# Performance work log

Hardware: AMD Instinct MI355X
Metric: run time of the kernel (lower is better)

## Reference

```python
import jax, jax.numpy as jnp
import numpy as np

B, N, C, H = 4, 2048, 256, 16
D = C // H  # head dim = 16


def setup_inputs() -> dict:
    key = jax.random.key(0)
    k1, k2, k3 = jax.random.split(key, 3)
    x = jax.random.normal(k1, (B, N, C), dtype=jnp.float32)
    w_qkv = jax.random.normal(k2, (C, 3 * C), dtype=jnp.float32) * (C ** -0.5)
    b_qkv = jnp.zeros((3 * C,), dtype=jnp.float32)
    w_proj = jax.random.normal(k3, (C, C), dtype=jnp.float32) * (C ** -0.5)
    b_proj = jnp.zeros((C,), dtype=jnp.float32)
    return {"x": x, "w_qkv": w_qkv, "b_qkv": b_qkv, "w_proj": w_proj, "b_proj": b_proj}


def reference(x, w_qkv, b_qkv, w_proj, b_proj):
    b, n, c = x.shape
    qkv = x @ w_qkv + b_qkv                       # (B, N, 3C)
    qkv = qkv.reshape(b, n, 3, H, D)
    q = jnp.transpose(qkv[:, :, 0], (0, 2, 1, 3))  # (B, H, N, D)
    k = jnp.transpose(qkv[:, :, 1], (0, 2, 1, 3))
    v = jnp.transpose(qkv[:, :, 2], (0, 2, 1, 3))
    # NOTE: the original module applies NO 1/sqrt(d) scaling.
    attn = jnp.einsum('bhqd,bhkd->bhqk', q, k)     # (B, H, N, N)
    attn = jax.nn.softmax(attn, axis=-1)
    out = jnp.einsum('bhqk,bhkd->bhqd', attn, v)   # (B, H, N, D)
    out = jnp.transpose(out, (0, 2, 1, 3)).reshape(b, n, c)
    return out @ w_proj + b_proj
```

## Files before the change

kernel.cpp:

```cpp
#include <hip/hip_runtime.h>
#include <stdint.h>

typedef __attribute__((ext_vector_type(8))) short short8;
typedef __attribute__((ext_vector_type(4))) short short4v;
typedef __attribute__((ext_vector_type(4))) float float4v;
typedef __attribute__((ext_vector_type(16))) float float16v;
typedef __attribute__((ext_vector_type(4))) uint32_t uint4v;

__device__ __forceinline__ short f2bf(float f) {
    union { float f; uint32_t u; } v; v.f = f;
    uint32_t u = v.u;
    uint32_t r = (u + 0x7fffu + ((u >> 16) & 1u)) >> 16;
    return (short)r;
}

#if __has_builtin(__builtin_amdgcn_cvt_pk_bf16_f32)
typedef __bf16 bf16x2_t __attribute__((ext_vector_type(2)));
__device__ __forceinline__ uint32_t cvt_pk2(float a, float b) {
    union { bf16x2_t v; uint32_t u; } c;
    c.v = __builtin_amdgcn_cvt_pk_bf16_f32(a, b);
    return c.u;
}
#else
__device__ __forceinline__ uint32_t cvt_pk2(float a, float b) {
    union { float f; uint32_t u; } x, y; x.f = a; y.f = b;
    return ((x.u + 0x8000u) >> 16) | ((y.u + 0x8000u) & 0xFFFF0000u);
}
#endif


__global__ __launch_bounds__(256) void cvtW_kernel(const float* __restrict__ wqkv,
                                                   const float* __restrict__ wproj,
                                                   short* __restrict__ outq,
                                                   short* __restrict__ outp) {
    int idx = blockIdx.x * 256 + threadIdx.x;
    if (idx < 196608) {
        int n = idx >> 8, k = idx & 255;
        outq[idx] = f2bf(wqkv[k * 768 + n]);
    } else {
        int i = idx - 196608;
        int n = i >> 8, k = i & 255;
        outp[i] = f2bf(wproj[k * 256 + n]);
    }
}


template<int MODE>
__global__ __launch_bounds__(256) void gemm_kernel(
    const void* __restrict__ Ap, const short* __restrict__ Bt,
    const float* __restrict__ bias,
    short* __restrict__ outQ, short* __restrict__ outK, short* __restrict__ outV,
    float* __restrict__ outP)
{
    const int K = 256;
    int m0 = blockIdx.x * 64;
    int n0 = blockIdx.y * 64;
    int tid = threadIdx.x;
    int wave = tid >> 6, lane = tid & 63, quad = lane >> 4, lc = lane & 15;

    __shared__ __align__(16) short As[64 * 48];
    __shared__ __align__(16) short Bs[64 * 48];

    float4v acc[4];
    #pragma unroll
    for (int t = 0; t < 4; ++t) acc[t] = (float4v){0.f, 0.f, 0.f, 0.f};

    int srow = tid >> 2, sseg = tid & 3;

    for (int c = 0; c < K; c += 32) {
        __syncthreads();
        if (MODE == 0) {
            const float* src = (const float*)Ap + (size_t)(m0 + srow) * K + c + sseg * 8;
            float4 f0 = *(const float4*)src;
            float4 f1 = *(const float4*)(src + 4);
            uint4v u; u.x = cvt_pk2(f0.x, f0.y); u.y = cvt_pk2(f0.z, f0.w);
            u.z = cvt_pk2(f1.x, f1.y); u.w = cvt_pk2(f1.z, f1.w);
            *(uint4v*)(&As[srow * 48 + sseg * 8]) = u;
        } else {
            *(short8*)(&As[srow * 48 + sseg * 8]) =
                *(const short8*)((const short*)Ap + (size_t)(m0 + srow) * K + c + sseg * 8);
        }
        *(short8*)(&Bs[srow * 48 + sseg * 8]) =
            *(const short8*)(Bt + (size_t)(n0 + srow) * K + c + sseg * 8);
        __syncthreads();

        short8 af = *(short8*)(&As[(wave * 16 + lc) * 48 + quad * 8]);
        #pragma unroll
        for (int t = 0; t < 4; ++t) {
            short8 bf = *(short8*)(&Bs[(t * 16 + lc) * 48 + quad * 8]);
            acc[t] = __builtin_amdgcn_mfma_f32_16x16x32_bf16(af, bf, acc[t], 0, 0, 0);
        }
    }

    #pragma unroll
    for (int t = 0; t < 4; ++t) {
        int cg = n0 + t * 16 + lc;
        float bv = bias[cg];
        #pragma unroll
        for (int r = 0; r < 4; ++r) {
            int rg = m0 + wave * 16 + quad * 4 + r;
            float val = acc[t][r] + bv;
            if (MODE == 0) {
                int s = cg >> 8, rem = cg & 255, h = rem >> 4, d = rem & 15;
                int b = rg >> 11, n = rg & 2047;
                if (s == 0) val *= 1.4426950408889634f;
                short* dst = (s == 0) ? outQ : ((s == 1) ? outK : outV);
                dst[((((size_t)b * 16 + h) * 2048 + n) << 4) + d] = f2bf(val);
            } else {
                outP[(size_t)rg * 256 + cg] = val;
            }
        }
    }
}


__global__ __launch_bounds__(256) void attn_kernel(
    const short* __restrict__ Q, const short* __restrict__ Kp, const short* __restrict__ V,
    short* __restrict__ Out)
{
    const int N = 2048;
    int bh = blockIdx.y;
    int b = bh >> 4, h = bh & 15;
    int tid = threadIdx.x;
    int wave = tid >> 6, lane = tid & 63;
    int m = lane & 31, hi = lane >> 5;
    int qbase = blockIdx.x * 128 + wave * 32;

    const short* Qh = Q + (size_t)bh * N * 16;
    const short* Kh = Kp + (size_t)bh * N * 16;
    const short* Vh = V + (size_t)bh * N * 16;

    __shared__ __align__(16) short Vt[32][264];

    {
        int r = 16 + (tid >> 4);
        int c0 = (tid & 15) * 16;
        short fill = (r == 16) ? (short)0x3F80 : (short)0;
        short8 f8;
        #pragma unroll
        for (int j = 0; j < 8; ++j) f8[j] = fill;
        *(short8*)(&Vt[r][c0]) = f8;
        *(short8*)(&Vt[r][c0 + 8]) = f8;
    }

    short8 qf = *(const short8*)(Qh + (size_t)(qbase + m) * 16 + hi * 8);

    float16v Oacc, zf;
    #pragma unroll
    for (int j = 0; j < 16; ++j) { Oacc[j] = 0.f; zf[j] = 0.f; }

    int sd = tid & 15, sa = tid >> 4;
    int kb = ((sa & 1) << 3) | (((sa >> 1) & 1) << 2) | ((sa >> 2) << 4);

    for (int sc = 0; sc < N; sc += 256) {
        __syncthreads();
        #pragma unroll
        for (int cc = 0; cc < 4; ++cc) {
            const short* vp = Vh + (size_t)(sc + cc * 64 + kb) * 16 + sd;
            short4v pack;
            pack.x = vp[0]; pack.y = vp[16]; pack.z = vp[32]; pack.w = vp[48];
            *(short4v*)(&Vt[sd][cc * 64 + sa * 4]) = pack;
        }
        __syncthreads();

        #pragma unroll
        for (int it = 0; it < 4; ++it) {
            int c = sc + it * 64;
            short8 kf1 = *(const short8*)(Kh + (size_t)(c + m) * 16 + hi * 8);
            short8 kf2 = *(const short8*)(Kh + (size_t)(c + 32 + m) * 16 + hi * 8);

            float16v S1 = __builtin_amdgcn_mfma_f32_32x32x16_bf16(kf1, qf, zf, 0, 0, 0);
            float16v S2 = __builtin_amdgcn_mfma_f32_32x32x16_bf16(kf2, qf, zf, 0, 0, 0);

            union { uint4v u; short8 s; } pA, pB, pC, pD;
            pA.u = (uint4v){
                cvt_pk2(__builtin_amdgcn_exp2f(S1[0]), __builtin_amdgcn_exp2f(S1[1])),
                cvt_pk2(__builtin_amdgcn_exp2f(S1[2]), __builtin_amdgcn_exp2f(S1[3])),
                cvt_pk2(__builtin_amdgcn_exp2f(S1[4]), __builtin_amdgcn_exp2f(S1[5])),
                cvt_pk2(__builtin_amdgcn_exp2f(S1[6]), __builtin_amdgcn_exp2f(S1[7]))};
            pB.u = (uint4v){
                cvt_pk2(__builtin_amdgcn_exp2f(S1[8]),  __builtin_amdgcn_exp2f(S1[9])),
                cvt_pk2(__builtin_amdgcn_exp2f(S1[10]), __builtin_amdgcn_exp2f(S1[11])),
                cvt_pk2(__builtin_amdgcn_exp2f(S1[12]), __builtin_amdgcn_exp2f(S1[13])),
                cvt_pk2(__builtin_amdgcn_exp2f(S1[14]), __builtin_amdgcn_exp2f(S1[15]))};
            pC.u = (uint4v){
                cvt_pk2(__builtin_amdgcn_exp2f(S2[0]), __builtin_amdgcn_exp2f(S2[1])),
                cvt_pk2(__builtin_amdgcn_exp2f(S2[2]), __builtin_amdgcn_exp2f(S2[3])),
                cvt_pk2(__builtin_amdgcn_exp2f(S2[4]), __builtin_amdgcn_exp2f(S2[5])),
                cvt_pk2(__builtin_amdgcn_exp2f(S2[6]), __builtin_amdgcn_exp2f(S2[7]))};
            pD.u = (uint4v){
                cvt_pk2(__builtin_amdgcn_exp2f(S2[8]),  __builtin_amdgcn_exp2f(S2[9])),
                cvt_pk2(__builtin_amdgcn_exp2f(S2[10]), __builtin_amdgcn_exp2f(S2[11])),
                cvt_pk2(__builtin_amdgcn_exp2f(S2[12]), __builtin_amdgcn_exp2f(S2[13])),
                cvt_pk2(__builtin_amdgcn_exp2f(S2[14]), __builtin_amdgcn_exp2f(S2[15]))};

            #pragma unroll
            for (int p = 0; p < 4; ++p) {
                short8 vf = *(const short8*)(&Vt[m][it * 64 + p * 16 + hi * 8]);
                short8 pf = (p == 0) ? pA.s : (p == 1) ? pB.s : (p == 2) ? pC.s : pD.s;
                Oacc = __builtin_amdgcn_mfma_f32_32x32x16_bf16(vf, pf, Oacc, 0, 0, 0);
            }
        }
    }

    float Lq = __shfl(Oacc[8], m, 64);
    float inv = 1.0f / Lq;
    uint32_t o0 = cvt_pk2(Oacc[0] * inv, Oacc[1] * inv);
    uint32_t o1 = cvt_pk2(Oacc[2] * inv, Oacc[3] * inv);
    uint32_t o2 = cvt_pk2(Oacc[4] * inv, Oacc[5] * inv);
    uint32_t o3 = cvt_pk2(Oacc[6] * inv, Oacc[7] * inv);
    short* row = Out + ((size_t)(b * 2048 + qbase + m)) * 256 + h * 16;
    uint2 w0; w0.x = o0; w0.y = o1;
    uint2 w1; w1.x = o2; w1.y = o3;
    *(uint2*)(row + hi * 4) = w0;
    *(uint2*)(row + 8 + hi * 4) = w1;
}


extern "C" void kernel_launch(void* const* d_in, const int* in_sizes, int n_in,
                              void* d_out, int out_size, void* d_ws, size_t ws_size,
                              hipStream_t stream) {
    const float* x      = (const float*)d_in[0];
    const float* w_qkv  = (const float*)d_in[1];
    const float* b_qkv  = (const float*)d_in[2];
    const float* w_proj = (const float*)d_in[3];
    const float* b_proj = (const float*)d_in[4];
    float* out = (float*)d_out;

    short* wqkvT  = (short*)d_ws;
    short* wprojT = wqkvT + 196608;
    short* Qb     = wprojT + 65536;
    short* Kb     = Qb + 2097152;
    short* Vb     = Kb + 2097152;
    short* Ab     = Vb + 2097152;

    cvtW_kernel<<<1024, 256, 0, stream>>>(w_qkv, w_proj, wqkvT, wprojT);

    gemm_kernel<0><<<dim3(128, 12), 256, 0, stream>>>(x, wqkvT, b_qkv, Qb, Kb, Vb, nullptr);

    attn_kernel<<<dim3(16, 64), 256, 0, stream>>>(Qb, Kb, Vb, Ab);

    gemm_kernel<1><<<dim3(128, 4), 256, 0, stream>>>(Ab, wprojT, b_proj,
                                                     nullptr, nullptr, nullptr, out);
}
```

Measured before the change: 139.9 us.

## Double GEMM M-tile to 128 rows and shrink attention V shared buffer

The projection GEMMs now compute 128 rows per block, with two 16-row subtiles per wave, so each B-tile load from shared memory is reused across twice as many MFMAs and the grid is halved. Separately, the attention kernel's transposed-V shared buffer drops from 32 to 17 rows: rows 16..31 of the 32x32 MFMA A operand, which held a ones row and zero padding, now all read the single ones row. This cuts LDS footprint and init stores. Rows 17..31 of the output then also accumulate row sums instead of zeros, but they are unused apart from row 16, which supplies the softmax denominator. Fewer GEMM blocks may reduce occupancy on a large-CU device.

```diff
diff --git a/kernel.cpp b/kernel.cpp
--- a/kernel.cpp
+++ b/kernel.cpp
@@ -53,58 +53,69 @@
     float* __restrict__ outP)
 {
     const int K = 256;
-    int m0 = blockIdx.x * 64;
+    int m0 = blockIdx.x * 128;
     int n0 = blockIdx.y * 64;
     int tid = threadIdx.x;
     int wave = tid >> 6, lane = tid & 63, quad = lane >> 4, lc = lane & 15;
 
-    __shared__ __align__(16) short As[64 * 48];
+    __shared__ __align__(16) short As[128 * 48];
     __shared__ __align__(16) short Bs[64 * 48];
 
-    float4v acc[4];
-    #pragma unroll
-    for (int t = 0; t < 4; ++t) acc[t] = (float4v){0.f, 0.f, 0.f, 0.f};
+    float4v acc[2][4];
+    #pragma unroll
+    for (int s = 0; s < 2; ++s)
+        #pragma unroll
+        for (int t = 0; t < 4; ++t) acc[s][t] = (float4v){0.f, 0.f, 0.f, 0.f};
 
     int srow = tid >> 2, sseg = tid & 3;
 
     for (int c = 0; c < K; c += 32) {
         __syncthreads();
-        if (MODE == 0) {
-            const float* src = (const float*)Ap + (size_t)(m0 + srow) * K + c + sseg * 8;
-            float4 f0 = *(const float4*)src;
-            float4 f1 = *(const float4*)(src + 4);
-            uint4v u; u.x = cvt_pk2(f0.x, f0.y); u.y = cvt_pk2(f0.z, f0.w);
-            u.z = cvt_pk2(f1.x, f1.y); u.w = cvt_pk2(f1.z, f1.w);
-            *(uint4v*)(&As[srow * 48 + sseg * 8]) = u;
-        } else {
-            *(short8*)(&As[srow * 48 + sseg * 8]) =
-                *(const short8*)((const short*)Ap + (size_t)(m0 + srow) * K + c + sseg * 8);
+        #pragma unroll
+        for (int s = 0; s < 2; ++s) {
+            int row = srow + s * 64;
+            if (MODE == 0) {
+                const float* src = (const float*)Ap + (size_t)(m0 + row) * K + c + sseg * 8;
+                float4 f0 = *(const float4*)src;
+                float4 f1 = *(const float4*)(src + 4);
+                uint4v u; u.x = cvt_pk2(f0.x, f0.y); u.y = cvt_pk2(f0.z, f0.w);
+                u.z = cvt_pk2(f1.x, f1.y); u.w = cvt_pk2(f1.z, f1.w);
+                *(uint4v*)(&As[row * 48 + sseg * 8]) = u;
+            } else {
+                *(short8*)(&As[row * 48 + sseg * 8]) =
+                    *(const short8*)((const short*)Ap + (size_t)(m0 + row) * K + c + sseg * 8);
+            }
         }
         *(short8*)(&Bs[srow * 48 + sseg * 8]) =
             *(const short8*)(Bt + (size_t)(n0 + srow) * K + c + sseg * 8);
         __syncthreads();
 
-        short8 af = *(short8*)(&As[(wave * 16 + lc) * 48 + quad * 8]);
-        #pragma unroll
-        for (int t = 0; t < 4; ++t) {
-            short8 bf = *(short8*)(&Bs[(t * 16 + lc) * 48 + quad * 8]);
-            acc[t] = __builtin_amdgcn_mfma_f32_16x16x32_bf16(af, bf, acc[t], 0, 0, 0);
-        }
-    }
-
+        #pragma unroll
+        for (int s = 0; s < 2; ++s) {
+            short8 af = *(short8*)(&As[(s * 64 + wave * 16 + lc) * 48 + quad * 8]);
+            #pragma unroll
+            for (int t = 0; t < 4; ++t) {
+                short8 bf = *(short8*)(&Bs[(t * 16 + lc) * 48 + quad * 8]);
+                acc[s][t] = __builtin_amdgcn_mfma_f32_16x16x32_bf16(af, bf, acc[s][t], 0, 0, 0);
+            }
+        }
+    }
+
+    #pragma unroll
+    for (int s = 0; s < 2; ++s)
     #pragma unroll
     for (int t = 0; t < 4; ++t) {
         int cg = n0 + t * 16 + lc;
         float bv = bias[cg];
         #pragma unroll
         for (int r = 0; r < 4; ++r) {
-            int rg = m0 + wave * 16 + quad * 4 + r;
-            float val = acc[t][r] + bv;
+            int rg = m0 + s * 64 + wave * 16 + quad * 4 + r;
+            float val = acc[s][t][r] + bv;
             if (MODE == 0) {
-                int s = cg >> 8, rem = cg & 255, h = rem >> 4, d = rem & 15;
+                int sq = cg >> 8, rem = cg & 255, h = rem >> 4, d = rem & 15;
                 int b = rg >> 11, n = rg & 2047;
-                if (s == 0) val *= 1.4426950408889634f;
-                short* dst = (s == 0) ? outQ : ((s == 1) ? outK : outV);
+                if (sq == 0) val *= 1.4426950408889634f;
+                short* dst = (sq == 0) ? outQ : ((sq == 1) ? outK : outV);
                 dst[((((size_t)b * 16 + h) * 2048 + n) << 4) + d] = f2bf(val);
             } else {
                 outP[(size_t)rg * 256 + cg] = val;
@@ -130,17 +141,14 @@
     const short* Kh = Kp + (size_t)bh * N * 16;
     const short* Vh = V + (size_t)bh * N * 16;
 
-    __shared__ __align__(16) short Vt[32][264];
-
-    {
-        int r = 16 + (tid >> 4);
-        int c0 = (tid & 15) * 16;
-        short fill = (r == 16) ? (short)0x3F80 : (short)0;
+    __shared__ __align__(16) short Vt[17][264];
+
+    if (tid < 16) {
         short8 f8;
         #pragma unroll
-        for (int j = 0; j < 8; ++j) f8[j] = fill;
-        *(short8*)(&Vt[r][c0]) = f8;
-        *(short8*)(&Vt[r][c0 + 8]) = f8;
+        for (int j = 0; j < 8; ++j) f8[j] = (short)0x3F80;
+        *(short8*)(&Vt[16][tid * 16]) = f8;
+        *(short8*)(&Vt[16][tid * 16 + 8]) = f8;
     }
 
     short8 qf = *(const short8*)(Qh + (size_t)(qbase + m) * 16 + hi * 8);
@@ -148,6 +156,8 @@
     float16v Oacc, zf;
     #pragma unroll
     for (int j = 0; j < 16; ++j) { Oacc[j] = 0.f; zf[j] = 0.f; }
+
+    int rEff = (m < 16) ? m : 16;
 
     int sd = tid & 15, sa = tid >> 4;
     int kb = ((sa & 1) << 3) | (((sa >> 1) & 1) << 2) | ((sa >> 2) << 4);
@@ -196,7 +206,7 @@
 
             #pragma unroll
             for (int p = 0; p < 4; ++p) {
-                short8 vf = *(const short8*)(&Vt[m][it * 64 + p * 16 + hi * 8]);
+                short8 vf = *(const short8*)(&Vt[rEff][it * 64 + p * 16 + hi * 8]);
                 short8 pf = (p == 0) ? pA.s : (p == 1) ? pB.s : (p == 2) ? pC.s : pD.s;
                 Oacc = __builtin_amdgcn_mfma_f32_32x32x16_bf16(vf, pf, Oacc, 0, 0, 0);
             }
@@ -236,10 +246,10 @@
 
     cvtW_kernel<<<1024, 256, 0, stream>>>(w_qkv, w_proj, wqkvT, wprojT);
 
-    gemm_kernel<0><<<dim3(128, 12), 256, 0, stream>>>(x, wqkvT, b_qkv, Qb, Kb, Vb, nullptr);
+    gemm_kernel<0><<<dim3(64, 12), 256, 0, stream>>>(x, wqkvT, b_qkv, Qb, Kb, Vb, nullptr);
 
     attn_kernel<<<dim3(16, 64), 256, 0, stream>>>(Qb, Kb, Vb, Ab);
 
-    gemm_kernel<1><<<dim3(128, 4), 256, 0, stream>>>(Ab, wprojT, b_proj,
-                                                     nullptr, nullptr, nullptr, out);
-}
+    gemm_kernel<1><<<dim3(64, 4), 256, 0, stream>>>(Ab, wprojT, b_proj,
+                                                    nullptr, nullptr, nullptr, out);
+}
```

After: 144.0 us. 3.0% more time.

## Keep A rows in registers and sweep N tiles per block in GEMMs

Applied to the files above, without the earlier changes.

The GEMM kernels now load each block's 64-row A strip once into registers as bf16 fragments, covering the full K. Each block then loops over several 64-wide N tiles, staging the full-K B tile in LDS and register-prefetching the next one. This replaces the 2D grid that reloaded and reconverted A once per N tile. In the attention kernel, the constant ones/zeros rows that were written to shared memory become register constants selected per lane, which halves the Vt LDS footprint. The trade-offs are fewer blocks (256), more register pressure, and a divergent select in the attention inner loop.

```diff
diff --git a/kernel.cpp b/kernel.cpp
--- a/kernel.cpp
+++ b/kernel.cpp
@@ -53,61 +53,88 @@
     float* __restrict__ outP)
 {
     const int K = 256;
-    int m0 = blockIdx.x * 64;
-    int n0 = blockIdx.y * 64;
+    const int NT = (MODE == 0) ? 6 : 2;
+    const int NSBASE = (MODE == 0) ? 384 : 128;
+    int bx = blockIdx.x;
+    int m0 = (bx >> 1) * 64;
+    int ns = bx & 1;
     int tid = threadIdx.x;
     int wave = tid >> 6, lane = tid & 63, quad = lane >> 4, lc = lane & 15;
 
-    __shared__ __align__(16) short As[64 * 48];
-    __shared__ __align__(16) short Bs[64 * 48];
-
-    float4v acc[4];
-    #pragma unroll
-    for (int t = 0; t < 4; ++t) acc[t] = (float4v){0.f, 0.f, 0.f, 0.f};
+    __shared__ __align__(16) short Bs[64 * 264];
+
+    short8 areg[8];
+    if (MODE == 0) {
+        const float* arow = (const float*)Ap + (size_t)(m0 + wave * 16 + lc) * K;
+        #pragma unroll
+        for (int ko = 0; ko < 8; ++ko) {
+            float4 f0 = *(const float4*)(arow + ko * 32 + quad * 8);
+            float4 f1 = *(const float4*)(arow + ko * 32 + quad * 8 + 4);
+            union { uint4v u; short8 s; } c;
+            c.u = (uint4v){cvt_pk2(f0.x, f0.y), cvt_pk2(f0.z, f0.w),
+                           cvt_pk2(f1.x, f1.y), cvt_pk2(f1.z, f1.w)};
+            areg[ko] = c.s;
+        }
+    } else {
+        const short* arow = (const short*)Ap + (size_t)(m0 + wave * 16 + lc) * K;
+        #pragma unroll
+        for (int ko = 0; ko < 8; ++ko)
+            areg[ko] = *(const short8*)(arow + ko * 32 + quad * 8);
+    }
 
     int srow = tid >> 2, sseg = tid & 3;
-
-    for (int c = 0; c < K; c += 32) {
-        __syncthreads();
-        if (MODE == 0) {
-            const float* src = (const float*)Ap + (size_t)(m0 + srow) * K + c + sseg * 8;
-            float4 f0 = *(const float4*)src;
-            float4 f1 = *(const float4*)(src + 4);
-            uint4v u; u.x = cvt_pk2(f0.x, f0.y); u.y = cvt_pk2(f0.z, f0.w);
-            u.z = cvt_pk2(f1.x, f1.y); u.w = cvt_pk2(f1.z, f1.w);
-            *(uint4v*)(&As[srow * 48 + sseg * 8]) = u;
-        } else {
-            *(short8*)(&As[srow * 48 + sseg * 8]) =
-                *(const short8*)((const short*)Ap + (size_t)(m0 + srow) * K + c + sseg * 8);
-        }
-        *(short8*)(&Bs[srow * 48 + sseg * 8]) =
-            *(const short8*)(Bt + (size_t)(n0 + srow) * K + c + sseg * 8);
-        __syncthreads();
-
-        short8 af = *(short8*)(&As[(wave * 16 + lc) * 48 + quad * 8]);
+    short8 breg[8];
+    {
+        const short* bsrc = Bt + (size_t)(ns * NSBASE + srow) * K + sseg * 64;
+        #pragma unroll
+        for (int k = 0; k < 8; ++k) breg[k] = *(const short8*)(bsrc + k * 8);
+    }
+
+    for (int j = 0; j < NT; ++j) {
+        __syncthreads();
+        {
+            short* bdst = &Bs[srow * 264 + sseg * 64];
+            #pragma unroll
+            for (int k = 0; k < 8; ++k) *(short8*)(bdst + k * 8) = breg[k];
+        }
+        if (j + 1 < NT) {
+            const short* bn = Bt + (size_t)(ns * NSBASE + (j + 1) * 64 + srow) * K + sseg * 64;
+            #pragma unroll
+            for (int k = 0; k < 8; ++k) breg[k] = *(const short8*)(bn + k * 8);
+        }
+        __syncthreads();
+
+        int n0 = ns * NSBASE + j * 64;
+        float4v acc[4];
+        #pragma unroll
+        for (int t = 0; t < 4; ++t) acc[t] = (float4v){0.f, 0.f, 0.f, 0.f};
+
+        #pragma unroll
+        for (int ko = 0; ko < 8; ++ko) {
+            #pragma unroll
+            for (int t = 0; t < 4; ++t) {
+                short8 bf = *(short8*)(&Bs[(t * 16 + lc) * 264 + ko * 32 + quad * 8]);
+                acc[t] = __builtin_amdgcn_mfma_f32_16x16x32_bf16(areg[ko], bf, acc[t], 0, 0, 0);
+            }
+        }
+
         #pragma unroll
         for (int t = 0; t < 4; ++t) {
-            short8 bf = *(short8*)(&Bs[(t * 16 + lc) * 48 + quad * 8]);
-            acc[t] = __builtin_amdgcn_mfma_f32_16x16x32_bf16(af, bf, acc[t], 0, 0, 0);
-        }
-    }
-
-    #pragma unroll
-    for (int t = 0; t < 4; ++t) {
-        int cg = n0 + t * 16 + lc;
-        float bv = bias[cg];
-        #pragma unroll
-        for (int r = 0; r < 4; ++r) {
-            int rg = m0 + wave * 16 + quad * 4 + r;
-            float val = acc[t][r] + bv;
-            if (MODE == 0) {
-                int s = cg >> 8, rem = cg & 255, h = rem >> 4, d = rem & 15;
-                int b = rg >> 11, n = rg & 2047;
-                if (s == 0) val *= 1.4426950408889634f;
-                short* dst = (s == 0) ? outQ : ((s == 1) ? outK : outV);
-                dst[((((size_t)b * 16 + h) * 2048 + n) << 4) + d] = f2bf(val);
-            } else {
-                outP[(size_t)rg * 256 + cg] = val;
+            int cg = n0 + t * 16 + lc;
+            float bv = bias[cg];
+            #pragma unroll
+            for (int r = 0; r < 4; ++r) {
+                int rg = m0 + wave * 16 + quad * 4 + r;
+                float val = acc[t][r] + bv;
+                if (MODE == 0) {
+                    int sq = cg >> 8, rem = cg & 255, h = rem >> 4, d = rem & 15;
+                    int b = rg >> 11, n = rg & 2047;
+                    if (sq == 0) val *= 1.4426950408889634f;
+                    short* dst = (sq == 0) ? outQ : ((sq == 1) ? outK : outV);
+                    dst[((((size_t)b * 16 + h) * 2048 + n) << 4) + d] = f2bf(val);
+                } else {
+                    outP[(size_t)rg * 256 + cg] = val;
+                }
             }
         }
     }
@@ -130,20 +157,13 @@
     const short* Kh = Kp + (size_t)bh * N * 16;
     const short* Vh = V + (size_t)bh * N * 16;
 
-    __shared__ __align__(16) short Vt[32][264];
-
-    {
-        int r = 16 + (tid >> 4);
-        int c0 = (tid & 15) * 16;
-        short fill = (r == 16) ? (short)0x3F80 : (short)0;
-        short8 f8;
-        #pragma unroll
-        for (int j = 0; j < 8; ++j) f8[j] = fill;
-        *(short8*)(&Vt[r][c0]) = f8;
-        *(short8*)(&Vt[r][c0 + 8]) = f8;
-    }
+    __shared__ __align__(16) short Vt[16][264];
 
     short8 qf = *(const short8*)(Qh + (size_t)(qbase + m) * 16 + hi * 8);
+
+    short8 ones, zeros;
+    #pragma unroll
+    for (int j = 0; j < 8; ++j) { ones[j] = (short)0x3F80; zeros[j] = 0; }
 
     float16v Oacc, zf;
     #pragma unroll
@@ -196,7 +216,10 @@
 
             #pragma unroll
             for (int p = 0; p < 4; ++p) {
-                short8 vf = *(const short8*)(&Vt[m][it * 64 + p * 16 + hi * 8]);
+                short8 vf;
+                if (m < 16)      vf = *(const short8*)(&Vt[m][it * 64 + p * 16 + hi * 8]);
+                else if (m == 16) vf = ones;
+                else              vf = zeros;
                 short8 pf = (p == 0) ? pA.s : (p == 1) ? pB.s : (p == 2) ? pC.s : pD.s;
                 Oacc = __builtin_amdgcn_mfma_f32_32x32x16_bf16(vf, pf, Oacc, 0, 0, 0);
             }
@@ -236,10 +259,10 @@
 
     cvtW_kernel<<<1024, 256, 0, stream>>>(w_qkv, w_proj, wqkvT, wprojT);
 
-    gemm_kernel<0><<<dim3(128, 12), 256, 0, stream>>>(x, wqkvT, b_qkv, Qb, Kb, Vb, nullptr);
+    gemm_kernel<0><<<256, 256, 0, stream>>>(x, wqkvT, b_qkv, Qb, Kb, Vb, nullptr);
 
     attn_kernel<<<dim3(16, 64), 256, 0, stream>>>(Qb, Kb, Vb, Ab);
 
-    gemm_kernel<1><<<dim3(128, 4), 256, 0, stream>>>(Ab, wprojT, b_proj,
-                                                     nullptr, nullptr, nullptr, out);
-}
+    gemm_kernel<1><<<256, 256, 0, stream>>>(Ab, wprojT, b_proj,
+                                            nullptr, nullptr, nullptr, out);
+}
```

Result: slower. 143.5 us (+2.6%).

## Split attention keys across two blocks with a float workspace combine kernel

Applied to the files above, without the earlier changes.

The attention kernel becomes a template that, when the workspace is large enough, splits the key range in half over a third grid dimension. Each half writes unnormalized output and row sums to a float workspace, and a new combine kernel adds the halves, normalizes and writes bf16. This doubles the block count (1024 to 2048) to fill more compute units, at the cost of an extra launch and workspace traffic. Separately, the shared-memory ones/zeros rows of the V tile are replaced by register constants chosen per lane, which shrinks shared memory but adds branches in the inner loop.

```diff
diff --git a/kernel.cpp b/kernel.cpp
--- a/kernel.cpp
+++ b/kernel.cpp
@@ -101,10 +101,10 @@
             int rg = m0 + wave * 16 + quad * 4 + r;
             float val = acc[t][r] + bv;
             if (MODE == 0) {
-                int s = cg >> 8, rem = cg & 255, h = rem >> 4, d = rem & 15;
+                int sq = cg >> 8, rem = cg & 255, h = rem >> 4, d = rem & 15;
                 int b = rg >> 11, n = rg & 2047;
-                if (s == 0) val *= 1.4426950408889634f;
-                short* dst = (s == 0) ? outQ : ((s == 1) ? outK : outV);
+                if (sq == 0) val *= 1.4426950408889634f;
+                short* dst = (sq == 0) ? outQ : ((sq == 1) ? outK : outV);
                 dst[((((size_t)b * 16 + h) * 2048 + n) << 4) + d] = f2bf(val);
             } else {
                 outP[(size_t)rg * 256 + cg] = val;
@@ -114,12 +114,15 @@
 }
 
 
+template<int SPLIT>
 __global__ __launch_bounds__(256) void attn_kernel(
     const short* __restrict__ Q, const short* __restrict__ Kp, const short* __restrict__ V,
-    short* __restrict__ Out)
+    short* __restrict__ Out, float* __restrict__ Pws)
 {
     const int N = 2048;
+    const int KEYS = N / SPLIT;
     int bh = blockIdx.y;
+    int half = (SPLIT == 2) ? blockIdx.z : 0;
     int b = bh >> 4, h = bh & 15;
     int tid = threadIdx.x;
     int wave = tid >> 6, lane = tid & 63;
@@ -130,20 +133,13 @@
     const short* Kh = Kp + (size_t)bh * N * 16;
     const short* Vh = V + (size_t)bh * N * 16;
 
-    __shared__ __align__(16) short Vt[32][264];
-
-    {
-        int r = 16 + (tid >> 4);
-        int c0 = (tid & 15) * 16;
-        short fill = (r == 16) ? (short)0x3F80 : (short)0;
-        short8 f8;
-        #pragma unroll
-        for (int j = 0; j < 8; ++j) f8[j] = fill;
-        *(short8*)(&Vt[r][c0]) = f8;
-        *(short8*)(&Vt[r][c0 + 8]) = f8;
-    }
+    __shared__ __align__(16) short Vt[16][264];
 
     short8 qf = *(const short8*)(Qh + (size_t)(qbase + m) * 16 + hi * 8);
+
+    short8 ones, zeros;
+    #pragma unroll
+    for (int j = 0; j < 8; ++j) { ones[j] = (short)0x3F80; zeros[j] = 0; }
 
     float16v Oacc, zf;
     #pragma unroll
@@ -152,7 +148,7 @@
     int sd = tid & 15, sa = tid >> 4;
     int kb = ((sa & 1) << 3) | (((sa >> 1) & 1) << 2) | ((sa >> 2) << 4);
 
-    for (int sc = 0; sc < N; sc += 256) {
+    for (int sc = half * KEYS; sc < (half + 1) * KEYS; sc += 256) {
         __syncthreads();
         #pragma unroll
         for (int cc = 0; cc < 4; ++cc) {
@@ -196,24 +192,61 @@
 
             #pragma unroll
             for (int p = 0; p < 4; ++p) {
-                short8 vf = *(const short8*)(&Vt[m][it * 64 + p * 16 + hi * 8]);
+                short8 vf;
+                if (m < 16)      vf = *(const short8*)(&Vt[m][it * 64 + p * 16 + hi * 8]);
+                else if (m == 16) vf = ones;
+                else              vf = zeros;
                 short8 pf = (p == 0) ? pA.s : (p == 1) ? pB.s : (p == 2) ? pC.s : pD.s;
                 Oacc = __builtin_amdgcn_mfma_f32_32x32x16_bf16(vf, pf, Oacc, 0, 0, 0);
             }
         }
     }
 
-    float Lq = __shfl(Oacc[8], m, 64);
-    float inv = 1.0f / Lq;
-    uint32_t o0 = cvt_pk2(Oacc[0] * inv, Oacc[1] * inv);
-    uint32_t o1 = cvt_pk2(Oacc[2] * inv, Oacc[3] * inv);
-    uint32_t o2 = cvt_pk2(Oacc[4] * inv, Oacc[5] * inv);
-    uint32_t o3 = cvt_pk2(Oacc[6] * inv, Oacc[7] * inv);
-    short* row = Out + ((size_t)(b * 2048 + qbase + m)) * 256 + h * 16;
-    uint2 w0; w0.x = o0; w0.y = o1;
-    uint2 w1; w1.x = o2; w1.y = o3;
-    *(uint2*)(row + hi * 4) = w0;
-    *(uint2*)(row + 8 + hi * 4) = w1;
+    if (SPLIT == 1) {
+        float Lq = __shfl(Oacc[8], m, 64);
+        float inv = 1.0f / Lq;
+        uint32_t o0 = cvt_pk2(Oacc[0] * inv, Oacc[1] * inv);
+        uint32_t o1 = cvt_pk2(Oacc[2] * inv, Oacc[3] * inv);
+        uint32_t o2 = cvt_pk2(Oacc[4] * inv, Oacc[5] * inv);
+        uint32_t o3 = cvt_pk2(Oacc[6] * inv, Oacc[7] * inv);
+        short* row = Out + ((size_t)(b * 2048 + qbase + m)) * 256 + h * 16;
+        uint2 w0; w0.x = o0; w0.y = o1;
+        uint2 w1; w1.x = o2; w1.y = o3;
+        *(uint2*)(row + hi * 4) = w0;
+        *(uint2*)(row + 8 + hi * 4) = w1;
+    } else {
+        float* base = Pws + (((size_t)half * 64 + bh) * 16 + blockIdx.x) * (17 * 128);
+        int ql = wave * 32 + m;
+        #pragma unroll
+        for (int r = 0; r < 8; ++r) {
+            int drow = (r & 3) + 8 * (r >> 2) + 4 * hi;
+            base[drow * 128 + ql] = Oacc[r];
+        }
+        if (hi == 0) base[16 * 128 + ql] = Oacc[8];
+    }
+}
+
+
+__global__ __launch_bounds__(256) void attn_combine(const float* __restrict__ Pws,
+                                                    short* __restrict__ Out) {
+    int qt = blockIdx.x, bh = blockIdx.y;
+    int b = bh >> 4, h = bh & 15;
+    const float* P1 = Pws + (((size_t)bh) * 16 + qt) * (17 * 128);
+    const float* P2 = P1 + (size_t)64 * 16 * 17 * 128;
+    int ql = threadIdx.x & 127, dh = threadIdx.x >> 7;
+    float L = P1[16 * 128 + ql] + P2[16 * 128 + ql];
+    float inv = 1.0f / L;
+    float v[8];
+    #pragma unroll
+    for (int j = 0; j < 8; ++j) {
+        int d = dh * 8 + j;
+        v[j] = (P1[d * 128 + ql] + P2[d * 128 + ql]) * inv;
+    }
+    union { uint4v u; short8 s; } c;
+    c.u = (uint4v){cvt_pk2(v[0], v[1]), cvt_pk2(v[2], v[3]),
+                   cvt_pk2(v[4], v[5]), cvt_pk2(v[6], v[7])};
+    int n = qt * 128 + ql;
+    *(short8*)(Out + ((size_t)(b * 2048 + n)) * 256 + h * 16 + dh * 8) = c.s;
 }
 
 
@@ -233,12 +266,21 @@
     short* Kb     = Qb + 2097152;
     short* Vb     = Kb + 2097152;
     short* Ab     = Vb + 2097152;
+    float* Pws    = (float*)(Ab + 2097152);
+    size_t needed = (size_t)(Ab + 2097152 - (short*)d_ws) * 2
+                  + (size_t)2 * 64 * 16 * 17 * 128 * 4;
+    bool split = ws_size >= needed;
 
     cvtW_kernel<<<1024, 256, 0, stream>>>(w_qkv, w_proj, wqkvT, wprojT);
 
     gemm_kernel<0><<<dim3(128, 12), 256, 0, stream>>>(x, wqkvT, b_qkv, Qb, Kb, Vb, nullptr);
 
-    attn_kernel<<<dim3(16, 64), 256, 0, stream>>>(Qb, Kb, Vb, Ab);
+    if (split) {
+        attn_kernel<2><<<dim3(16, 64, 2), 256, 0, stream>>>(Qb, Kb, Vb, Ab, Pws);
+        attn_combine<<<dim3(16, 64), 256, 0, stream>>>(Pws, Ab);
+    } else {
+        attn_kernel<1><<<dim3(16, 64), 256, 0, stream>>>(Qb, Kb, Vb, Ab, nullptr);
+    }
 
     gemm_kernel<1><<<dim3(128, 4), 256, 0, stream>>>(Ab, wprojT, b_proj,
                                                      nullptr, nullptr, nullptr, out);
```

Measured after the change: 140.9 us. No clear change (+0.8%).
